# Performance work log

Hardware: AMD Instinct MI355X
Metric: run time of the kernel (lower is better)

The kernel has to match this reference:

```python
import jax, jax.numpy as jnp
import numpy as np

SIG = 512                                   # sigSize
NA = 45                                     # numAngles
SQRT2 = float(np.sqrt(2.0))
DIAG = int(np.ceil(SQRT2 * SIG))            # 725, padded (circle=False) size
PAD = int(np.ceil(SQRT2 * SIG - SIG))       # 213
PAD_BEFORE = (SIG + PAD) // 2 - SIG // 2    # 106
THETA = jnp.asarray(np.deg2rad(np.linspace(0.0, 180.0, NA, endpoint=False)), dtype=jnp.float32)


def _rotate_all(img):
    """Bilinear grid_sample rotation (align_corners=True, zero padding) for all angles.
    img: (B, D, D) -> (B, A, D, D)."""
    D = img.shape[-1]
    c = jnp.linspace(-1.0, 1.0, D, dtype=img.dtype)
    xg = c[None, None, :]                    # column coord j
    yg = c[None, :, None]                    # row coord i
    ct = jnp.cos(THETA)[:, None, None]
    st = jnp.sin(THETA)[:, None, None]
    # affine_grid with R = [[c, s, 0], [-s, c, 0]]
    xs = ct * xg + st * yg                   # (A, D, D)
    ys = -st * xg + ct * yg
    px = (xs + 1.0) * 0.5 * (D - 1)
    py = (ys + 1.0) * 0.5 * (D - 1)
    x0 = jnp.floor(px)
    y0 = jnp.floor(py)
    wx = px - x0
    wy = py - y0
    x0i = x0.astype(jnp.int32)
    y0i = y0.astype(jnp.int32)

    def tap(xi, yi, w):
        valid = (xi >= 0) & (xi < D) & (yi >= 0) & (yi < D)
        xi = jnp.clip(xi, 0, D - 1)
        yi = jnp.clip(yi, 0, D - 1)
        return img[:, yi, xi] * (w * valid)[None]

    return (tap(x0i, y0i, (1 - wx) * (1 - wy)) + tap(x0i + 1, y0i, wx * (1 - wy))
            + tap(x0i, y0i + 1, (1 - wx) * wy) + tap(x0i + 1, y0i + 1, wx * wy))


def radon(x):
    """fmult: x (B,1,S,S) -> sinogram (B,1,D,A), circle=False."""
    xp = jnp.pad(x[:, 0], ((0, 0), (PAD_BEFORE, PAD - PAD_BEFORE), (PAD_BEFORE, PAD - PAD_BEFORE)))
    rot = _rotate_all(xp)                    # (B, A, D, D)
    sino = rot.sum(axis=2)                   # ray-sum over rows -> (B, A, D)
    return jnp.transpose(sino, (0, 2, 1))[:, None]   # (B, 1, D, A)


def iradon(sino):
    """ftran: unfiltered backprojection. sino (B,1,D,A) -> (B,1,S,S)."""
    B, _, D, A = sino.shape
    c = jnp.linspace(-1.0, 1.0, D, dtype=sino.dtype)
    ct = jnp.cos(THETA)[:, None, None]
    st = jnp.sin(THETA)[:, None, None]
    t = ct * c[None, None, :] - st * c[None, :, None]     # (A, D, D) detector coord
    pt = (t + 1.0) * 0.5 * (D - 1)
    t0 = jnp.floor(pt)
    wt = pt - t0
    t0i = t0.astype(jnp.int32)
    s = jnp.transpose(sino[:, 0], (0, 2, 1))               # (B, A, D)

    def tap(ti, w):
        valid = (ti >= 0) & (ti < D)
        tic = jnp.clip(ti, 0, D - 1)
        v = jnp.take_along_axis(s, tic.reshape(1, A, D * D), axis=2).reshape(B, A, D, D)
        return v * (w * valid)[None]

    acc = tap(t0i, 1.0 - wt) + tap(t0i + 1, wt)
    reco = acc.sum(axis=1)                                 # sum over angles
    reco = reco[:, PAD_BEFORE:PAD_BEFORE + SIG, PAD_BEFORE:PAD_BEFORE + SIG]
    return (reco * (jnp.pi / (2.0 * A)))[:, None]


def setup_inputs() -> dict:
    key = jax.random.key(0)
    k1, k2 = jax.random.split(key)
    x = jax.random.normal(k1, (2, 1, SIG, SIG), dtype=jnp.float32)
    y = jax.random.normal(k2, (2, 1, DIAG, NA), dtype=jnp.float32)
    return {"x": x, "y": y}


def reference(x, y):
    # CTClass.grad: per-sample ftran(fmult(x_i) - y_i), vectorized over batch
    return iradon(radon(x) - y)
```

## Files before the change

kernel.cpp:

```cpp
#include <hip/hip_runtime.h>
#include <math.h>

#define SIG 512
#define NA 45
#define DD 725
#define PB 106
#define HALFF 362.0f
#define PI_D 3.14159265358979323846

#define TD2 32
#define TY2 32
#define NT2 23
#define NC42 13
#define RW2 52
#define RH2 47
#define NREG2 640
#define NTILES2 (2 * NA * NT2 * NT2)
#define TGRP (NT2 * NT2)

#define ZSTR 728
#define ZELEMS (2 * NA * ZSTR)
#define TBLOFF ZELEMS
#define DESCOFF 65616
#define DESCI 12
#define BMOFF (DESCOFF + NTILES2 * DESCI)
#define BMWORDS 1492
#define WS_NEED ((BMOFF + BMWORDS) * 4)
#define WS_TBL ((TBLOFF + 2 * NA) * 4)

#define NZB 256
#define NSB 186

#define SEGW2 32

__device__ __forceinline__ float cidx(int i) {
    return -1.0f + (float)i * (2.0f / 724.0f);
}

__device__ __forceinline__ void ref_trig(int a, float& ct, float& st) {
    float thf = (float)((double)(4 * a) * PI_D / 180.0);
    ct = (float)cos((double)thf);
    st = (float)sin((double)thf);
}

__device__ __forceinline__ bool tile_geom(
    int a, int b, int td, int ty, float ct, float st,
    int& dlohi, int& gcb, int& grb, int& nrows, int& kske, int& y0i,
    int& zbase, int& boff, float& pxbase, float& pybase) {
    float X0 = HALFF * (1.0f - ct - st);
    float Y0 = HALFF * (1.0f + st - ct);
    int d0 = td * TD2, dmax = min(d0 + TD2 - 1, DD - 1);
    int y0 = ty * TY2, ymax = min(y0 + TY2 - 1, DD - 1);
    const float lo = (float)(PB - 1), hi = (float)(PB + SIG);

    float Ax0 = fmaf(ct, (float)d0, X0), Ax1 = fmaf(ct, (float)dmax, X0);
    float Axlo = fminf(Ax0, Ax1), Axhi = fmaxf(Ax0, Ax1);
    float Ay0 = fmaf(-st, (float)d0, Y0), Ay1 = fmaf(-st, (float)dmax, Y0);
    float Aylo = fminf(Ay0, Ay1), Ayhi = fmaxf(Ay0, Ay1);
    float ylo = (float)y0, yhi = (float)ymax;
    if (st > 1e-6f) {
        ylo = fmaxf(ylo, (lo - Axhi) / st - 1.0f);
        yhi = fminf(yhi, (hi - Axlo) / st + 1.0f);
    } else if (Axhi <= lo || Axlo >= hi) { return false; }
    if (ct > 1e-6f) {
        ylo = fmaxf(ylo, (lo - Ayhi) / ct - 1.0f);
        yhi = fminf(yhi, (hi - Aylo) / ct + 1.0f);
    } else if (ct < -1e-6f) {
        ylo = fmaxf(ylo, (hi - Aylo) / ct - 1.0f);
        yhi = fminf(yhi, (lo - Ayhi) / ct + 1.0f);
    } else if (Ayhi <= lo || Aylo >= hi) { return false; }
    int yclo = max(y0, (int)ceilf(ylo));
    int ychi = min(ymax, (int)floorf(yhi));
    if (ychi < yclo) return false;
    float yclof = (float)yclo, ychif = (float)ychi;

    float dloF = (float)d0, dhiF = (float)dmax;
    if (ct > 1e-6f) {
        dloF = fmaxf(dloF, (lo - st * ychif - X0) / ct - 1.0f);
        dhiF = fminf(dhiF, (hi - st * yclof - X0) / ct + 1.0f);
    } else if (ct < -1e-6f) {
        dloF = fmaxf(dloF, (hi - st * yclof - X0) / ct - 1.0f);
        dhiF = fminf(dhiF, (lo - st * ychif - X0) / ct + 1.0f);
    }
    if (st > 1e-6f) {
        float yl2 = (ct >= 0.0f) ? yclof : ychif;
        float yh2 = (ct >= 0.0f) ? ychif : yclof;
        dloF = fmaxf(dloF, (Y0 + ct * yl2 - hi) / st - 1.0f);
        dhiF = fminf(dhiF, (Y0 + ct * yh2 - lo) / st + 1.0f);
    }
    int dclo = max(d0, (int)ceilf(dloF));
    int dchi = min(dmax, (int)floorf(dhiF));
    if (dchi < dclo) return false;

    float pxmin = 1e30f, pxmax = -1e30f, pymin = 1e30f, pymax = -1e30f;
    for (int ci = 0; ci < 4; ++ci) {
        float df = (float)((ci & 1) ? dchi : dclo);
        float yf = (float)((ci & 2) ? ychi : yclo);
        float px = fmaf(st, yf, fmaf(ct, df, X0));
        float py = fmaf(ct, yf, fmaf(-st, df, Y0));
        pxmin = fminf(pxmin, px); pxmax = fmaxf(pxmax, px);
        pymin = fminf(pymin, py); pymax = fmaxf(pymax, py);
    }
    int cx0 = (int)floorf(pxmin) - 1;
    int cx1 = (int)floorf(pxmax) + 2;
    int ry0 = (int)floorf(pymin) - 1;
    int ry1 = (int)floorf(pymax) + 2;
    if (cx1 < PB || cx0 >= PB + SIG || ry1 < PB || ry0 >= PB + SIG) return false;

    int cx0a = PB + (((cx0 - PB) >> 2) << 2);
    nrows = min(ry1 - ry0 + 1, RH2);
    gcb = cx0a - PB;
    grb = ry0 - PB;
    dlohi = (dclo - d0) | ((dchi - d0) << 8);
    kske = (yclo - y0) | ((ychi - y0) << 8);
    y0i = y0;
    zbase = (b * NA + a) * ZSTR + 1 + d0;
    boff = b * SIG * SIG;
    pxbase = fmaf(ct, (float)d0, X0) - (float)cx0a;
    pybase = fmaf(-st, (float)d0, Y0) - (float)ry0;
    return true;
}

template <int MODE>
__global__ void prep(const float* __restrict__ yin, float* __restrict__ z,
                     float* __restrict__ tbl, float* __restrict__ zpage,
                     int* __restrict__ desc, unsigned* __restrict__ bmap) {
    __shared__ float s_trig[4];
    __shared__ int s_ag[2];
    if (blockIdx.x < NZB) {
        int i = blockIdx.x * blockDim.x + threadIdx.x;
        if (i < 256) zpage[i] = 0.0f;
        if (MODE >= 1 && blockIdx.x == 0 && threadIdx.x < NA) {
            float ct, st;
            ref_trig(threadIdx.x, ct, st);
            tbl[2 * threadIdx.x] = ct;
            tbl[2 * threadIdx.x + 1] = st;
        }
        if (i >= ZELEMS) return;
        int r = i / ZSTR;
        int c = i - r * ZSTR;
        float v = 0.0f;
        if (c >= 1 && c <= DD) {
            int d = c - 1;
            int a = r % NA;
            int b = r / NA;
            v = -yin[(b * DD + d) * NA + a];
        }
        z[i] = v;
        return;
    }
    if (MODE < 2) return;
    int base = (blockIdx.x - NZB) * blockDim.x;
    if (threadIdx.x < 2) {
        int tl = min(base + (int)threadIdx.x * 255, NTILES2 - 1);
        int ag = tl / TGRP;
        s_ag[threadIdx.x] = ag;
        float ct, st;
        ref_trig(ag % NA, ct, st);
        s_trig[2 * threadIdx.x] = ct;
        s_trig[2 * threadIdx.x + 1] = st;
    }
    __syncthreads();
    int tile = base + threadIdx.x;
    bool live = false;
    int dlohi, gcb, grb, nrows, kske, y0i, zbase, boff;
    float pxbase, pybase;
    float ct = 0.0f, st = 0.0f;
    if (tile < NTILES2) {
        int td = tile % NT2; int rest = tile / NT2;
        int ty = rest % NT2;
        int ag = rest / NT2;
        int a = ag % NA;
        int b = ag / NA;
        int sel = (ag == s_ag[0]) ? 0 : 2;
        ct = s_trig[sel]; st = s_trig[sel + 1];
        live = tile_geom(a, b, td, ty, ct, st, dlohi, gcb, grb, nrows, kske,
                         y0i, zbase, boff, pxbase, pybase);
    }
    unsigned long long m = __ballot(live);
    if ((threadIdx.x & 63) == 0) {
        int w = tile >> 5;
        bmap[w] = (unsigned)m;
        bmap[w + 1] = (unsigned)(m >> 32);
    }
    if (!live) return;
    {
        int nch = (nrows * NC42 + 63) >> 6;
        int rmax = (nch * 64 - 1) / NC42;
        if (grb >= 0 && grb + rmax < SIG && gcb >= 0 && gcb + 52 <= SIG)
            dlohi |= (1 << 16);
    }
    int* dp = desc + tile * DESCI;
    float* fp = (float*)dp;
    dp[0] = dlohi; dp[1] = gcb; dp[2] = grb; dp[3] = nrows;
    dp[4] = kske; fp[5] = pxbase; fp[6] = pybase;
    dp[7] = y0i; dp[8] = zbase; dp[9] = boff;
    fp[10] = ct; fp[11] = st;
}

__device__ __forceinline__ void process_tile32(
    const float* __restrict__ img, const float* __restrict__ zpage,
    float ct, float st,
    int dlohi, int gcb, int grb, int nrows, int kske, int y0i, int zbase,
    float pxbase, float pybase,
    float4* reg4, float* __restrict__ z) {
    float* reg = (float*)reg4;
    int lane = threadIdx.x;

    int nch = (nrows * NC42 + 63) >> 6;
    if (dlohi & (1 << 16)) {
        int r0 = (lane * 5) >> 6;
        int c0 = lane - r0 * NC42;
        const float* src = img + ((grb + r0) << 9) + gcb + (c0 << 2);
        for (int ch = 0; ch < nch; ++ch) {
            __builtin_amdgcn_global_load_lds(
                (const __attribute__((address_space(1))) void*)src,
                (__attribute__((address_space(3))) void*)(reg4 + (ch << 6)),
                16, 0, 0);
            bool cy = (c0 != 0);
            src += cy ? (5 * SIG - 4) : (4 * SIG + 48);
            c0 = cy ? (c0 - 1) : (NC42 - 1);
        }
    } else {
        for (int ch = 0; ch < nch; ++ch) {
            int vi = (ch << 6) + lane;
            int r = vi / NC42;
            int c = vi - r * NC42;
            int gr = grb + r;
            int gc = gcb + (c << 2);
            bool valid = ((unsigned)gr < SIG) & ((unsigned)gc < SIG);
            const float* src = valid ? (img + (gr << 9) + gc) : zpage;
            __builtin_amdgcn_global_load_lds(
                (const __attribute__((address_space(1))) void*)src,
                (__attribute__((address_space(3))) void*)(reg4 + (ch << 6)),
                16, 0, 0);
        }
    }
    __syncthreads();

    int half = lane >> 5;
    int dl = lane & 31;
    int ksb = kske & 255, keb = kske >> 8;
    int dlo = dlohi & 255, dhi = (dlohi >> 8) & 255;
    int n = keb - ksb + 1;
    int sq = ksb + ((n * half) >> 1);
    int eq = ksb + ((n * (half + 1)) >> 1) - 1;

    float lf = (float)min(max(dl, dlo), dhi);
    float pxd = fmaf(ct, lf, pxbase);
    float pyd = fmaf(-st, lf, pybase);
    float yif = (float)(y0i + sq);
    float px = fmaf(st, yif, pxd);
    float py = fmaf(ct, yif, pyd);
    float sum = 0.0f;
#pragma unroll 4
    for (int k = sq; k <= eq; ++k) {
        float fx = floorf(px), fy = floorf(py);
        float wx = px - fx, wy = py - fy;
        int addr = (int)fmaf(fy, (float)RW2, fx);
        float v00 = reg[addr],       v10 = reg[addr + 1];
        float v01 = reg[addr + RW2], v11 = reg[addr + RW2 + 1];
        float top = fmaf(wx, v10 - v00, v00);
        float bot = fmaf(wx, v11 - v01, v01);
        sum = fmaf(wy, bot - top, sum + top);
        px += st; py += ct;
    }
    sum += __shfl_xor(sum, 32);
    if (half == 0 && dl >= dlo && dl <= dhi) {
        atomicAdd(&z[zbase + dl], sum);
    }
}

__global__ __launch_bounds__(64) void radon32f(const float* __restrict__ x,
                                               const float* __restrict__ zpage,
                                               const int* __restrict__ desc,
                                               const unsigned* __restrict__ bmap,
                                               float* __restrict__ z) {
    __shared__ float4 reg4[NREG2];
    unsigned w = bmap[blockIdx.x >> 5];
    if (!((w >> (blockIdx.x & 31)) & 1u)) return;
    const int* dp = desc + blockIdx.x * DESCI;
    const float* fp = (const float*)dp;
    process_tile32(x + dp[9], zpage, fp[10], fp[11],
                   dp[0], dp[1], dp[2], dp[3], dp[4], dp[7], dp[8],
                   fp[5], fp[6], reg4, z);
}

template <int TBL>
__global__ __launch_bounds__(64) void radon32(const float* __restrict__ x,
                                              const float* __restrict__ zpage,
                                              const float* __restrict__ tbl,
                                              float* __restrict__ z) {
    __shared__ float4 reg4[NREG2];
    int tile = blockIdx.x;
    int td = tile % NT2; int rest = tile / NT2;
    int ty = rest % NT2; rest /= NT2;
    int a = rest % NA;
    int b = rest / NA;
    float ct, st;
    if (TBL) { ct = tbl[2 * a]; st = tbl[2 * a + 1]; }
    else     { ref_trig(a, ct, st); }
    int dlohi, gcb, grb, nrows, kske, y0i, zbase, boff;
    float pxbase, pybase;
    if (!tile_geom(a, b, td, ty, ct, st, dlohi, gcb, grb, nrows, kske, y0i,
                   zbase, boff, pxbase, pybase)) return;
    process_tile32(x + boff, zpage, ct, st, dlohi, gcb, grb, nrows, kske,
                   y0i, zbase, pxbase, pybase, reg4, z);
}

template <int TBL>
__global__ __launch_bounds__(256) void iradon16(const float* __restrict__ z,
                                                const float* __restrict__ tbl,
                                                float* __restrict__ out) {
    __shared__ float s_sc[NA], s_st2[NA];
    __shared__ int s_lo[NA];
    __shared__ float s_B[NA * 16];
    __shared__ float s_seg[NA * SEGW2];

    int t = threadIdx.x;
    int b = blockIdx.x >> 10;
    int tb = blockIdx.x & 1023;
    int i0 = (tb >> 5) << 4;
    int j0 = (tb & 31) << 4;

    if (t < NA) {
        float ct, st;
        if (TBL) { ct = tbl[2 * t]; st = tbl[2 * t + 1]; }
        else     { ref_trig(t, ct, st); }
        float sc = ct * HALFF;
        float st2 = -st * HALFF;
        float cxl = cidx(j0 + PB), cxh = cidx(j0 + 15 + PB);
        float cyl = cidx(i0 + PB), cyh = cidx(i0 + 15 + PB);
        float a00 = fmaf(sc, cxl, fmaf(st2, cyl, 363.0f));
        float a01 = fmaf(sc, cxl, fmaf(st2, cyh, 363.0f));
        float a10 = fmaf(sc, cxh, fmaf(st2, cyl, 363.0f));
        float a11 = fmaf(sc, cxh, fmaf(st2, cyh, 363.0f));
        float mn = fminf(fminf(a00, a01), fminf(a10, a11));
        int lo = (int)floorf(mn) - 1;
        lo = min(max(lo, 0), ZSTR - 1 - SEGW2);
        s_sc[t] = sc; s_st2[t] = st2; s_lo[t] = lo;
    }
    __syncthreads();

    for (int s = t; s < NA * 16; s += 256) {
        int a = s >> 4, ii = s & 15;
        s_B[s] = fmaf(s_st2[a], cidx(i0 + ii + PB), 363.0f - (float)s_lo[a]);
    }
    const float* zb = z + b * NA * ZSTR;
    for (int s = t; s < NA * SEGW2; s += 256) {
        int a = s >> 5, idx = s & 31;
        s_seg[s] = zb[a * ZSTR + s_lo[a] + idx];
    }
    __syncthreads();

    float cxv = cidx(j0 + (t & 15) + PB);
    int r0 = t >> 4;
    float acc = 0.f;
    for (int a = 0; a < NA; ++a) {
        float af = fmaf(s_sc[a], cxv, s_B[(a << 4) + r0]);
        float fl = floorf(af);
        float wt = af - fl;
        int ia = min(max((int)af, 0), SEGW2 - 2);
        float v0 = s_seg[(a << 5) + ia], v1 = s_seg[(a << 5) + ia + 1];
        acc = fmaf(wt, v1 - v0, acc + v0);
    }
    const float sfin = (float)(PI_D / (2.0 * NA));
    out[(b << 18) + ((i0 + r0) << 9) + j0 + (t & 15)] = acc * sfin;
}

extern "C" void kernel_launch(void* const* d_in, const int* in_sizes, int n_in,
                              void* d_out, int out_size, void* d_ws, size_t ws_size,
                              hipStream_t stream) {
    const float* x = (const float*)d_in[0];
    const float* yin = (const float*)d_in[1];
    float* out = (float*)d_out;
    float* z = (float*)d_ws;
    float* tbl = z + TBLOFF;
    int* desc = (int*)(z + DESCOFF);
    unsigned* bmap = (unsigned*)(z + BMOFF);
    float* zpage = out;

    if (ws_size >= (size_t)WS_NEED) {
        prep<2><<<NZB + NSB, 256, 0, stream>>>(yin, z, tbl, zpage, desc, bmap);
        radon32f<<<NTILES2, 64, 0, stream>>>(x, zpage, desc, bmap, z);
        iradon16<1><<<2048, 256, 0, stream>>>(z, tbl, out);
    } else if (ws_size >= (size_t)WS_TBL) {
        prep<1><<<NZB, 256, 0, stream>>>(yin, z, tbl, zpage, nullptr, nullptr);
        radon32<1><<<NTILES2, 64, 0, stream>>>(x, zpage, tbl, z);
        iradon16<1><<<2048, 256, 0, stream>>>(z, tbl, out);
    } else {
        prep<0><<<NZB, 256, 0, stream>>>(yin, z, nullptr, zpage, nullptr, nullptr);
        radon32<0><<<NTILES2, 64, 0, stream>>>(x, zpage, nullptr, z);
        iradon16<0><<<2048, 256, 0, stream>>>(z, nullptr, out);
    }
}
```

Baseline: 40.43 us.

## Enlarge radon tiles to 48 rows with 64-wide LDS rows; drop clamp in backprojection

Changes the radon tile from 32x32 to 32 detectors by 48 ray-steps, so there are fewer tiles and the staged image region is 64 floats wide (16 float4 per row). This makes the LDS load indexing shift-based instead of division-based and cuts per-tile descriptor, setup and atomic overhead. The cost is a larger LDS footprint per block (16 KB), which may lower occupancy, and more wasted halo loads. Separately, the backprojection drops the clamp on the segment index, which relies on the geometry keeping it in range.

```diff
diff --git a/kernel.cpp b/kernel.cpp
--- a/kernel.cpp
+++ b/kernel.cpp
@@ -9,14 +9,15 @@
 #define PI_D 3.14159265358979323846
 
 #define TD2 32
-#define TY2 32
-#define NT2 23
-#define NC42 13
-#define RW2 52
-#define RH2 47
-#define NREG2 640
-#define NTILES2 (2 * NA * NT2 * NT2)
-#define TGRP (NT2 * NT2)
+#define TY2 48
+#define NTD 23
+#define NTY 16
+#define NC42 16
+#define RW2 64
+#define RH2 61
+#define NREG2 1024
+#define NTILES2 (2 * NA * NTD * NTY)
+#define TGRP (NTD * NTY)
 
 #define ZSTR 728
 #define ZELEMS (2 * NA * ZSTR)
@@ -24,12 +25,12 @@
 #define DESCOFF 65616
 #define DESCI 12
 #define BMOFF (DESCOFF + NTILES2 * DESCI)
-#define BMWORDS 1492
+#define BMWORDS 1040
 #define WS_NEED ((BMOFF + BMWORDS) * 4)
 #define WS_TBL ((TBLOFF + 2 * NA) * 4)
 
 #define NZB 256
-#define NSB 186
+#define NSB 130
 
 #define SEGW2 32
 
@@ -167,9 +168,9 @@
     float pxbase, pybase;
     float ct = 0.0f, st = 0.0f;
     if (tile < NTILES2) {
-        int td = tile % NT2; int rest = tile / NT2;
-        int ty = rest % NT2;
-        int ag = rest / NT2;
+        int td = tile % NTD; int rest = tile / NTD;
+        int ty = rest % NTY;
+        int ag = rest / NTY;
         int a = ag % NA;
         int b = ag / NA;
         int sel = (ag == s_ag[0]) ? 0 : 2;
@@ -185,9 +186,9 @@
     }
     if (!live) return;
     {
-        int nch = (nrows * NC42 + 63) >> 6;
-        int rmax = (nch * 64 - 1) / NC42;
-        if (grb >= 0 && grb + rmax < SIG && gcb >= 0 && gcb + 52 <= SIG)
+        int nch = (nrows + 3) >> 2;
+        int rmax = 4 * nch - 1;
+        if (grb >= 0 && grb + rmax < SIG && gcb >= 0 && gcb + 64 <= SIG)
             dlohi |= (1 << 16);
     }
     int* dp = desc + tile * DESCI;
@@ -207,25 +208,23 @@
     float* reg = (float*)reg4;
     int lane = threadIdx.x;
 
-    int nch = (nrows * NC42 + 63) >> 6;
+    int nch = (nrows + 3) >> 2;
     if (dlohi & (1 << 16)) {
-        int r0 = (lane * 5) >> 6;
-        int c0 = lane - r0 * NC42;
+        int r0 = lane >> 4;
+        int c0 = lane & 15;
         const float* src = img + ((grb + r0) << 9) + gcb + (c0 << 2);
         for (int ch = 0; ch < nch; ++ch) {
             __builtin_amdgcn_global_load_lds(
                 (const __attribute__((address_space(1))) void*)src,
                 (__attribute__((address_space(3))) void*)(reg4 + (ch << 6)),
                 16, 0, 0);
-            bool cy = (c0 != 0);
-            src += cy ? (5 * SIG - 4) : (4 * SIG + 48);
-            c0 = cy ? (c0 - 1) : (NC42 - 1);
+            src += 4 * SIG;
         }
     } else {
         for (int ch = 0; ch < nch; ++ch) {
             int vi = (ch << 6) + lane;
-            int r = vi / NC42;
-            int c = vi - r * NC42;
+            int r = vi >> 4;
+            int c = vi & 15;
             int gr = grb + r;
             int gc = gcb + (c << 2);
             bool valid = ((unsigned)gr < SIG) & ((unsigned)gc < SIG);
@@ -271,11 +270,11 @@
     }
 }
 
-__global__ __launch_bounds__(64) void radon32f(const float* __restrict__ x,
-                                               const float* __restrict__ zpage,
-                                               const int* __restrict__ desc,
-                                               const unsigned* __restrict__ bmap,
-                                               float* __restrict__ z) {
+__global__ __launch_bounds__(64) void radon48(const float* __restrict__ x,
+                                              const float* __restrict__ zpage,
+                                              const int* __restrict__ desc,
+                                              const unsigned* __restrict__ bmap,
+                                              float* __restrict__ z) {
     __shared__ float4 reg4[NREG2];
     unsigned w = bmap[blockIdx.x >> 5];
     if (!((w >> (blockIdx.x & 31)) & 1u)) return;
@@ -293,8 +292,8 @@
                                               float* __restrict__ z) {
     __shared__ float4 reg4[NREG2];
     int tile = blockIdx.x;
-    int td = tile % NT2; int rest = tile / NT2;
-    int ty = rest % NT2; rest /= NT2;
+    int td = tile % NTD; int rest = tile / NTD;
+    int ty = rest % NTY; rest /= NTY;
     int a = rest % NA;
     int b = rest / NA;
     float ct, st;
@@ -304,6 +303,12 @@
     float pxbase, pybase;
     if (!tile_geom(a, b, td, ty, ct, st, dlohi, gcb, grb, nrows, kske, y0i,
                    zbase, boff, pxbase, pybase)) return;
+    {
+        int nch = (nrows + 3) >> 2;
+        int rmax = 4 * nch - 1;
+        if (grb >= 0 && grb + rmax < SIG && gcb >= 0 && gcb + 64 <= SIG)
+            dlohi |= (1 << 16);
+    }
     process_tile32(x + boff, zpage, ct, st, dlohi, gcb, grb, nrows, kske,
                    y0i, zbase, pxbase, pybase, reg4, z);
 }
@@ -360,8 +365,9 @@
         float af = fmaf(s_sc[a], cxv, s_B[(a << 4) + r0]);
         float fl = floorf(af);
         float wt = af - fl;
-        int ia = min(max((int)af, 0), SEGW2 - 2);
-        float v0 = s_seg[(a << 5) + ia], v1 = s_seg[(a << 5) + ia + 1];
+        int ia = (int)fl;
+        const float* sp = s_seg + (a << 5) + ia;
+        float v0 = sp[0], v1 = sp[1];
         acc = fmaf(wt, v1 - v0, acc + v0);
     }
     const float sfin = (float)(PI_D / (2.0 * NA));
@@ -382,7 +388,7 @@
 
     if (ws_size >= (size_t)WS_NEED) {
         prep<2><<<NZB + NSB, 256, 0, stream>>>(yin, z, tbl, zpage, desc, bmap);
-        radon32f<<<NTILES2, 64, 0, stream>>>(x, zpage, desc, bmap, z);
+        radon48<<<NTILES2, 64, 0, stream>>>(x, zpage, desc, bmap, z);
         iradon16<1><<<2048, 256, 0, stream>>>(z, tbl, out);
     } else if (ws_size >= (size_t)WS_TBL) {
         prep<1><<<NZB, 256, 0, stream>>>(yin, z, tbl, zpage, nullptr, nullptr);
```

Result: slower. 51.25 us (+26.8%).
